# Kernel tuning notes

Measured on AMD Instinct MI355X. Metric: run time of the kernel, lower is better.

## Reference

```python
import jax, jax.numpy as jnp
import numpy as np

N_TOKENS = 32768
D_MODEL = 1024
TOT_EXPERT = 16
TOP_K = 2


def setup_inputs() -> dict:
    key = jax.random.key(0)
    k1, k2 = jax.random.split(key)
    inp = jax.random.normal(k1, (N_TOKENS, D_MODEL), dtype=jnp.float32)
    # nn.Linear(d_model, tot_expert, bias=False) weight: [tot_expert, d_model]
    W = jax.random.normal(k2, (TOT_EXPERT, D_MODEL), dtype=jnp.float32) * 0.02
    return {"inp": inp, "W": W}


def reference(inp, W):
    # gate logits: [N, E]
    logits = jnp.einsum('nd,ed->ne', inp, W)
    # top-k over experts (sorted order differs from torch sorted=False, but the
    # selected set and the downstream math are identical)
    top_k_logits, top_k_indices = jax.lax.top_k(logits, TOP_K)  # [N, K]
    # scatter top-k logits into a -inf buffer, then softmax over experts
    rows = jnp.arange(inp.shape[0])[:, None]
    router = jnp.full_like(logits, -jnp.inf).at[rows, top_k_indices].set(top_k_logits)
    router_probs = jax.nn.softmax(router, axis=-1)  # [N, E]
    # load-balance loss: f_i (no-grad expert selection freq) dot P_i (mean prob)
    f_i = jnp.zeros((TOT_EXPERT,), jnp.float32).at[top_k_indices.reshape(-1)].add(1.0) / inp.shape[0]
    P_i = jnp.mean(router_probs.astype(jnp.float32), axis=0)
    loss = jnp.sum(jax.lax.stop_gradient(f_i) * P_i) * TOT_EXPERT
    # gather the softmaxed scores of the selected experts
    top_k_scores = jnp.take_along_axis(router_probs, top_k_indices, axis=-1)  # [N, K]
    return top_k_indices, top_k_scores, loss
```

## Files before the change

kernel.cpp:

```cpp
#include <hip/hip_runtime.h>
#include <math.h>

#define N_TOKENS 32768
#define D_MODEL  1024
#define N_EXPERT 16
#define TPB      256
#define NBLK     512
#define TOKS     64
#define BATCH    16

typedef float f32x4 __attribute__((ext_vector_type(4)));
typedef float f32x2 __attribute__((ext_vector_type(2)));

template<int CTRL>
static __device__ __forceinline__ float dpp_xor(float v) {
    return __int_as_float(__builtin_amdgcn_update_dpp(
        0, __float_as_int(v), CTRL, 0xF, 0xF, true));
}

static __device__ __forceinline__ float dot4pk(f32x4 x, f32x4 w) {
    f32x2 xl = __builtin_shufflevector(x, x, 0, 1);
    f32x2 xh = __builtin_shufflevector(x, x, 2, 3);
    f32x2 wl = __builtin_shufflevector(w, w, 0, 1);
    f32x2 wh = __builtin_shufflevector(w, w, 2, 3);
    f32x2 m, r;
    asm("v_pk_mul_f32 %0, %1, %2" : "=v"(m) : "v"(xl), "v"(wl));
    asm("v_pk_fma_f32 %0, %1, %2, %3" : "=v"(r) : "v"(xh), "v"(wh), "v"(m));
    return r.x + r.y;
}


__global__ __launch_bounds__(256, 3)
void gate_kernel(const float* __restrict__ inp,
                 const float* __restrict__ W,
                 float* __restrict__ out,
                 float* __restrict__ ws)
{
    const int tid  = threadIdx.x;
    const int wave = tid >> 6;
    const int lane = tid & 63;
    const int p    = lane & 15;
    const int d0   = wave * 256 + lane * 4;
    const int base = blockIdx.x * TOKS;

    f32x4 wreg[N_EXPERT];
    #pragma unroll
    for (int j = 0; j < N_EXPERT; ++j)
        wreg[j] = *reinterpret_cast<const f32x4*>(W + (j ^ p) * D_MODEL + d0);

    __shared__ float lds_part[2][BATCH][4][N_EXPERT];
    __shared__ float lds_red[4][2][N_EXPERT];

    float cnt_acc = 0.f;
    float ps_acc  = 0.f;

#define LOADX(xr, t) xr = *reinterpret_cast<const f32x4*>(xptr + (t) * D_MODEL);

#define DOTOK(xv, t, BUF) do { \
    float a0 =dot4pk(xv,wreg[0]),  a1 =dot4pk(xv,wreg[1]);  \
    float a2 =dot4pk(xv,wreg[2]),  a3 =dot4pk(xv,wreg[3]);  \
    float a4 =dot4pk(xv,wreg[4]),  a5 =dot4pk(xv,wreg[5]);  \
    float a6 =dot4pk(xv,wreg[6]),  a7 =dot4pk(xv,wreg[7]);  \
    float a8 =dot4pk(xv,wreg[8]),  a9 =dot4pk(xv,wreg[9]);  \
    float a10=dot4pk(xv,wreg[10]), a11=dot4pk(xv,wreg[11]); \
    float a12=dot4pk(xv,wreg[12]), a13=dot4pk(xv,wreg[13]); \
    float a14=dot4pk(xv,wreg[14]), a15=dot4pk(xv,wreg[15]); \
    float b0 = a0 + dpp_xor<0x128>(a8);  \
    float b1 = a1 + dpp_xor<0x128>(a9);  \
    float b2 = a2 + dpp_xor<0x128>(a10); \
    float b3 = a3 + dpp_xor<0x128>(a11); \
    float b4 = a4 + dpp_xor<0x128>(a12); \
    float b5 = a5 + dpp_xor<0x128>(a13); \
    float b6 = a6 + dpp_xor<0x128>(a14); \
    float b7 = a7 + dpp_xor<0x128>(a15); \
    float c0 = b0 + __shfl_xor(b4, 4); \
    float c1 = b1 + __shfl_xor(b5, 4); \
    float c2 = b2 + __shfl_xor(b6, 4); \
    float c3 = b3 + __shfl_xor(b7, 4); \
    float d0_ = c0 + dpp_xor<0x4E>(c2); \
    float d1_ = c1 + dpp_xor<0x4E>(c3); \
    float s0  = d0_ + dpp_xor<0xB1>(d1_); \
    s0 += __shfl_xor(s0, 16); \
    s0 += __shfl_xor(s0, 32); \
    if (lane < N_EXPERT) BUF[t][wave][lane] = s0; \
} while (0)

    for (int b = 0; b < TOKS / BATCH; ++b) {
        const int tb0 = base + b * BATCH;
        const float* xptr = inp + (size_t)tb0 * D_MODEL + d0;
        float (*buf)[4][N_EXPERT] = lds_part[b & 1];

        f32x4 x0, x1, x2, x3;
        LOADX(x0, 0) LOADX(x1, 1) LOADX(x2, 2) LOADX(x3, 3)
        for (int g = 0; g < 3; ++g) {
            const int t = g * 4;
            DOTOK(x0, t + 0, buf); LOADX(x0, t + 4)
            DOTOK(x1, t + 1, buf); LOADX(x1, t + 5)
            DOTOK(x2, t + 2, buf); LOADX(x2, t + 6)
            DOTOK(x3, t + 3, buf); LOADX(x3, t + 7)
        }
        DOTOK(x0, 12, buf); DOTOK(x1, 13, buf);
        DOTOK(x2, 14, buf); DOTOK(x3, 15, buf);

        __syncthreads();

        {
            const int tgrp = tid >> 4;
            const int el   = tid & 15;
            float v1 = buf[tgrp][0][el] + buf[tgrp][1][el]
                     + buf[tgrp][2][el] + buf[tgrp][3][el];
            int   i1 = el;
            float v2 = -INFINITY;
            int   i2 = 0;
            #pragma unroll
            for (int m = 1; m <= 8; m <<= 1) {
                float o1 = __shfl_xor(v1, m);
                int  oi1 = __shfl_xor(i1, m);
                float o2 = __shfl_xor(v2, m);
                int  oi2 = __shfl_xor(i2, m);
                bool afirst = (v1 > o1) || (v1 == o1 && i1 < oi1);
                float c1v = afirst ? v1 : o1;   int c1i = afirst ? i1 : oi1;
                float bv  = afirst ? o1 : v1;   int bi  = afirst ? oi1 : i1;
                float sv  = afirst ? v2 : o2;   int si  = afirst ? i2 : oi2;
                bool sgt  = (bv > sv) || (bv == sv && bi < si);
                v1 = c1v; i1 = c1i;
                v2 = sgt ? bv : sv;  i2 = sgt ? bi : si;
            }
            float tt = expf(v2 - v1);
            float p1 = 1.f / (1.f + tt);
            float p2 = tt * p1;
            const int tok = tb0 + tgrp;
            if (el == 0) {
                *reinterpret_cast<float2*>(out + 2 * tok) =
                    make_float2((float)i1, (float)i2);
                *reinterpret_cast<float2*>(out + 2 * N_TOKENS + 2 * tok) =
                    make_float2(p1, p2);
            }
            cnt_acc += (el == i1 ? 1.f : 0.f) + (el == i2 ? 1.f : 0.f);
            ps_acc  += (el == i1 ? p1  : 0.f) + (el == i2 ? p2  : 0.f);
        }
    }

    cnt_acc += __shfl_xor(cnt_acc, 16); cnt_acc += __shfl_xor(cnt_acc, 32);
    ps_acc  += __shfl_xor(ps_acc, 16);  ps_acc  += __shfl_xor(ps_acc, 32);
    if (lane < N_EXPERT) {
        lds_red[wave][0][lane] = cnt_acc;
        lds_red[wave][1][lane] = ps_acc;
    }
    __syncthreads();
    if (tid < 32) {
        const int el = tid & 15;
        const int which = tid >> 4;
        float v = lds_red[0][which][el] + lds_red[1][which][el]
                + lds_red[2][which][el] + lds_red[3][which][el];
        ws[blockIdx.x * 32 + tid] = v;
    }
#undef LOADX
#undef DOTOK
}

__global__ void loss_kernel(const float* __restrict__ ws, float* __restrict__ out)
{
    __shared__ float partial[8][32];
    __shared__ float col[32];
    const int tid = threadIdx.x;
    const int c   = tid & 31;
    const int ch  = tid >> 5;
    float s0 = 0.f, s1 = 0.f, s2 = 0.f, s3 = 0.f;
    for (int b = 0; b < NBLK / 8; b += 4) {
        s0 += ws[(size_t)(ch * (NBLK / 8) + b + 0) * 32 + c];
        s1 += ws[(size_t)(ch * (NBLK / 8) + b + 1) * 32 + c];
        s2 += ws[(size_t)(ch * (NBLK / 8) + b + 2) * 32 + c];
        s3 += ws[(size_t)(ch * (NBLK / 8) + b + 3) * 32 + c];
    }
    partial[ch][c] = (s0 + s1) + (s2 + s3);
    __syncthreads();
    if (tid < 32) {
        float t = 0.f;
        #pragma unroll
        for (int k = 0; k < 8; ++k) t += partial[k][tid];
        col[tid] = t;
    }
    __syncthreads();
    if (tid == 0) {
        float sum = 0.f;
        #pragma unroll
        for (int e = 0; e < N_EXPERT; ++e)
            sum += col[e] * col[16 + e];
        out[4 * N_TOKENS] = sum * (float)N_EXPERT
                          / ((float)N_TOKENS * (float)N_TOKENS);
    }
}

extern "C" void kernel_launch(void* const* d_in, const int* in_sizes, int n_in,
                              void* d_out, int out_size, void* d_ws, size_t ws_size,
                              hipStream_t stream)
{
    const float* inp = (const float*)d_in[0];
    const float* W   = (const float*)d_in[1];
    float* out = (float*)d_out;
    float* ws  = (float*)d_ws;

    gate_kernel<<<NBLK, TPB, 0, stream>>>(inp, W, out, ws);
    loss_kernel<<<1, 256, 0, stream>>>(ws, out);
}
```

Baseline: 39.01 us.

## Halve tokens per block and prefetch next batch across the reduction barrier

Each block now handles 32 tokens instead of 64, doubling the grid to 1024 blocks and raising the occupancy hint to 4 blocks per CU. The two 16-token batches are fully unrolled, and the first loads of the second batch are issued before the barrier and top-2 reduction of the first batch, so memory latency overlaps that phase. The loss kernel now reduces twice as many per-block partials, and the higher occupancy target may limit registers for the 64-register weight cache.

```diff
diff --git a/kernel.cpp b/kernel.cpp
--- a/kernel.cpp
+++ b/kernel.cpp
@@ -5,8 +5,8 @@
 #define D_MODEL  1024
 #define N_EXPERT 16
 #define TPB      256
-#define NBLK     512
-#define TOKS     64
+#define NBLK     1024
+#define TOKS     32
 #define BATCH    16
 
 typedef float f32x4 __attribute__((ext_vector_type(4)));
@@ -30,7 +30,7 @@
 }
 
 
-__global__ __launch_bounds__(256, 3)
+__global__ __launch_bounds__(256, 4)
 void gate_kernel(const float* __restrict__ inp,
                  const float* __restrict__ W,
                  float* __restrict__ out,
@@ -54,9 +54,11 @@
     float cnt_acc = 0.f;
     float ps_acc  = 0.f;
 
-#define LOADX(xr, t) xr = *reinterpret_cast<const f32x4*>(xptr + (t) * D_MODEL);
-
-#define DOTOK(xv, t, BUF) do { \
+    const float* xptr = inp + (size_t)base * D_MODEL + d0;
+
+#define LOADX(xr, t) xr = *reinterpret_cast<const f32x4*>(xptr + (size_t)(t) * D_MODEL);
+
+#define DOTOK(xv, slot, BUF) do { \
     float a0 =dot4pk(xv,wreg[0]),  a1 =dot4pk(xv,wreg[1]);  \
     float a2 =dot4pk(xv,wreg[2]),  a3 =dot4pk(xv,wreg[3]);  \
     float a4 =dot4pk(xv,wreg[4]),  a5 =dot4pk(xv,wreg[5]);  \
@@ -82,67 +84,81 @@
     float s0  = d0_ + dpp_xor<0xB1>(d1_); \
     s0 += __shfl_xor(s0, 16); \
     s0 += __shfl_xor(s0, 32); \
-    if (lane < N_EXPERT) BUF[t][wave][lane] = s0; \
+    if (lane < N_EXPERT) BUF[slot][wave][lane] = s0; \
 } while (0)
 
-    for (int b = 0; b < TOKS / BATCH; ++b) {
-        const int tb0 = base + b * BATCH;
-        const float* xptr = inp + (size_t)tb0 * D_MODEL + d0;
-        float (*buf)[4][N_EXPERT] = lds_part[b & 1];
-
-        f32x4 x0, x1, x2, x3;
-        LOADX(x0, 0) LOADX(x1, 1) LOADX(x2, 2) LOADX(x3, 3)
-        for (int g = 0; g < 3; ++g) {
-            const int t = g * 4;
-            DOTOK(x0, t + 0, buf); LOADX(x0, t + 4)
-            DOTOK(x1, t + 1, buf); LOADX(x1, t + 5)
-            DOTOK(x2, t + 2, buf); LOADX(x2, t + 6)
-            DOTOK(x3, t + 3, buf); LOADX(x3, t + 7)
-        }
-        DOTOK(x0, 12, buf); DOTOK(x1, 13, buf);
-        DOTOK(x2, 14, buf); DOTOK(x3, 15, buf);
-
-        __syncthreads();
-
-        {
-            const int tgrp = tid >> 4;
-            const int el   = tid & 15;
-            float v1 = buf[tgrp][0][el] + buf[tgrp][1][el]
-                     + buf[tgrp][2][el] + buf[tgrp][3][el];
-            int   i1 = el;
-            float v2 = -INFINITY;
-            int   i2 = 0;
-            #pragma unroll
-            for (int m = 1; m <= 8; m <<= 1) {
-                float o1 = __shfl_xor(v1, m);
-                int  oi1 = __shfl_xor(i1, m);
-                float o2 = __shfl_xor(v2, m);
-                int  oi2 = __shfl_xor(i2, m);
-                bool afirst = (v1 > o1) || (v1 == o1 && i1 < oi1);
-                float c1v = afirst ? v1 : o1;   int c1i = afirst ? i1 : oi1;
-                float bv  = afirst ? o1 : v1;   int bi  = afirst ? oi1 : i1;
-                float sv  = afirst ? v2 : o2;   int si  = afirst ? i2 : oi2;
-                bool sgt  = (bv > sv) || (bv == sv && bi < si);
-                v1 = c1v; i1 = c1i;
-                v2 = sgt ? bv : sv;  i2 = sgt ? bi : si;
-            }
-            float tt = expf(v2 - v1);
-            float p1 = 1.f / (1.f + tt);
-            float p2 = tt * p1;
-            const int tok = tb0 + tgrp;
-            if (el == 0) {
-                *reinterpret_cast<float2*>(out + 2 * tok) =
-                    make_float2((float)i1, (float)i2);
-                *reinterpret_cast<float2*>(out + 2 * N_TOKENS + 2 * tok) =
-                    make_float2(p1, p2);
-            }
-            cnt_acc += (el == i1 ? 1.f : 0.f) + (el == i2 ? 1.f : 0.f);
-            ps_acc  += (el == i1 ? p1  : 0.f) + (el == i2 ? p2  : 0.f);
-        }
-    }
+#define PHASEB(BUF, TOKBASE) do { \
+    const int tgrp = tid >> 4; \
+    const int el   = tid & 15; \
+    float v1 = BUF[tgrp][0][el] + BUF[tgrp][1][el] \
+             + BUF[tgrp][2][el] + BUF[tgrp][3][el]; \
+    int   i1 = el; \
+    float v2 = -INFINITY; \
+    int   i2 = 0; \
+    _Pragma("unroll") \
+    for (int m = 1; m <= 8; m <<= 1) { \
+        float o1 = __shfl_xor(v1, m); \
+        int  oi1 = __shfl_xor(i1, m); \
+        float o2 = __shfl_xor(v2, m); \
+        int  oi2 = __shfl_xor(i2, m); \
+        bool afirst = (v1 > o1) || (v1 == o1 && i1 < oi1); \
+        float c1v = afirst ? v1 : o1;   int c1i = afirst ? i1 : oi1; \
+        float bv  = afirst ? o1 : v1;   int bi  = afirst ? oi1 : i1; \
+        float sv  = afirst ? v2 : o2;   int si  = afirst ? i2 : oi2; \
+        bool sgt  = (bv > sv) || (bv == sv && bi < si); \
+        v1 = c1v; i1 = c1i; \
+        v2 = sgt ? bv : sv;  i2 = sgt ? bi : si; \
+    } \
+    float tt = expf(v2 - v1); \
+    float p1 = 1.f / (1.f + tt); \
+    float p2 = tt * p1; \
+    const int tok = (TOKBASE) + tgrp; \
+    if (el == 0) { \
+        *reinterpret_cast<float2*>(out + 2 * tok) = \
+            make_float2((float)i1, (float)i2); \
+        *reinterpret_cast<float2*>(out + 2 * N_TOKENS + 2 * tok) = \
+            make_float2(p1, p2); \
+    } \
+    cnt_acc += (el == i1 ? 1.f : 0.f) + (el == i2 ? 1.f : 0.f); \
+    ps_acc  += (el == i1 ? p1  : 0.f) + (el == i2 ? p2  : 0.f); \
+} while (0)
+
+    f32x4 x0, x1, x2, x3;
+
+    LOADX(x0, 0) LOADX(x1, 1) LOADX(x2, 2) LOADX(x3, 3)
+    for (int g = 0; g < 3; ++g) {
+        const int t = g * 4;
+        DOTOK(x0, t + 0, lds_part[0]); LOADX(x0, t + 4)
+        DOTOK(x1, t + 1, lds_part[0]); LOADX(x1, t + 5)
+        DOTOK(x2, t + 2, lds_part[0]); LOADX(x2, t + 6)
+        DOTOK(x3, t + 3, lds_part[0]); LOADX(x3, t + 7)
+    }
+    DOTOK(x0, 12, lds_part[0]); LOADX(x0, 16)
+    DOTOK(x1, 13, lds_part[0]); LOADX(x1, 17)
+    DOTOK(x2, 14, lds_part[0]); LOADX(x2, 18)
+    DOTOK(x3, 15, lds_part[0]); LOADX(x3, 19)
+
+    __syncthreads();
+    PHASEB(lds_part[0], base);
+
+    for (int g = 0; g < 3; ++g) {
+        const int t = 16 + g * 4;
+        DOTOK(x0, (t + 0) & 15, lds_part[1]); LOADX(x0, t + 4)
+        DOTOK(x1, (t + 1) & 15, lds_part[1]); LOADX(x1, t + 5)
+        DOTOK(x2, (t + 2) & 15, lds_part[1]); LOADX(x2, t + 6)
+        DOTOK(x3, (t + 3) & 15, lds_part[1]); LOADX(x3, t + 7)
+    }
+    DOTOK(x0, 12, lds_part[1]);
+    DOTOK(x1, 13, lds_part[1]);
+    DOTOK(x2, 14, lds_part[1]);
+    DOTOK(x3, 15, lds_part[1]);
+
+    __syncthreads();
+    PHASEB(lds_part[1], base + 16);
 
     cnt_acc += __shfl_xor(cnt_acc, 16); cnt_acc += __shfl_xor(cnt_acc, 32);
     ps_acc  += __shfl_xor(ps_acc, 16);  ps_acc  += __shfl_xor(ps_acc, 32);
+    __syncthreads();
     if (lane < N_EXPERT) {
         lds_red[wave][0][lane] = cnt_acc;
         lds_red[wave][1][lane] = ps_acc;
@@ -157,6 +173,7 @@
     }
 #undef LOADX
 #undef DOTOK
+#undef PHASEB
 }
 
 __global__ void loss_kernel(const float* __restrict__ ws, float* __restrict__ out)
```

Result: faster. 37.71 us (-3.3%).
